# Kernel tuning notes

Measured on AMD Instinct MI355X. Metric: run time of the kernel, lower is better.

Reference implementation:

```python
import jax, jax.numpy as jnp
import numpy as np

N = 100000      # nodes
E = 3200000     # edges (avg degree 32)
F_IN = 16       # node_feature_size
R1, R2, R3 = 8, 16, 8   # gcn hidden sizes
N1 = 32                  # mlp hidden


def _lin(k, fan_in, shape):
    s = 1.0 / np.sqrt(fan_in)
    return jax.random.uniform(k, shape, minval=-s, maxval=s, dtype=jnp.float32)


def setup_inputs() -> dict:
    key = jax.random.key(0)
    ks = jax.random.split(key, 16)
    x = jax.random.normal(ks[0], (N, F_IN), dtype=jnp.float32)
    edge_index = jax.random.randint(ks[1], (2, E), 0, N, dtype=jnp.int64)
    return {
        "x": x,
        "edge_index": edge_index,
        # GraphConv k: out = mean_agg(x_j) @ W_rel + b + x @ W_root  (PyG GraphConv, lin_root bias=False)
        "W_rel1": _lin(ks[2], F_IN, (F_IN, R1)), "b1": _lin(ks[3], F_IN, (R1,)), "W_root1": _lin(ks[4], F_IN, (F_IN, R1)),
        "W_rel2": _lin(ks[5], R1, (R1, R2)),   "b2": _lin(ks[6], R1, (R2,)),   "W_root2": _lin(ks[7], R1, (R1, R2)),
        "W_rel3": _lin(ks[8], R2, (R2, R3)),   "b3": _lin(ks[9], R2, (R3,)),   "W_root3": _lin(ks[10], R2, (R2, R3)),
        "fc1_W": _lin(ks[11], R3, (R3, N1)), "fc1_b": _lin(ks[12], R3, (N1,)),
        "fc2_W": _lin(ks[13], N1, (N1, 1)),  "fc2_b": _lin(ks[14], N1, (1,)),
    }


def _graph_conv(x, src, dst, W_rel, b, W_root):
    # message: gather source features; aggregate: mean over incoming edges at dst
    n = x.shape[0]
    msg_sum = jax.ops.segment_sum(x[src], dst, num_segments=n)          # [N, F]
    cnt = jax.ops.segment_sum(jnp.ones(src.shape, x.dtype), dst, num_segments=n)
    mean = msg_sum / jnp.maximum(cnt, 1.0)[:, None]
    return mean @ W_rel + b + x @ W_root


def reference(x, edge_index, W_rel1, b1, W_root1, W_rel2, b2, W_root2,
              W_rel3, b3, W_root3, fc1_W, fc1_b, fc2_W, fc2_b):
    src, dst = edge_index[0], edge_index[1]
    h = jax.nn.sigmoid(_graph_conv(x, src, dst, W_rel1, b1, W_root1))
    h = jax.nn.sigmoid(_graph_conv(h, src, dst, W_rel2, b2, W_root2))
    h = jax.nn.sigmoid(_graph_conv(h, src, dst, W_rel3, b3, W_root3))
    h = jax.nn.sigmoid(h @ fc1_W + fc1_b)
    return h @ fc2_W + fc2_b   # [N, 1]
```

## Files before the change

kernel.cpp:

```cpp
#include <hip/hip_runtime.h>
#include <math.h>


#define CHUNK  8192
#define BW     128
#define MAXB   6144
#define MAXNB  800
#define MAXBLK 512

typedef _Float16 half8 __attribute__((ext_vector_type(8)));

static __device__ __forceinline__ float sigmoidf_(float x) {
    return 1.0f / (1.0f + expf(-x));
}

static __device__ __forceinline__ int scan256_excl(int v, int* s) {
    int tid = threadIdx.x;
    s[tid] = v;
    for (int off = 1; off < 256; off <<= 1) {
        __syncthreads();
        int t = (tid >= off) ? s[tid - off] : 0;
        __syncthreads();
        s[tid] += t;
    }
    __syncthreads();
    return s[tid] - v;
}

static __device__ __forceinline__ void gather_mean8(
    const half8* __restrict__ t, const int* __restrict__ csr,
    int rs, int d, float* s) {
#pragma unroll
    for (int c = 0; c < 8; ++c) s[c] = 0.0f;
    int e = 0;
    for (; e + 4 <= d; e += 4) {
        int4 ci = *(const int4*)(csr + rs + e);
        half8 v0 = t[ci.x]; half8 v1 = t[ci.y];
        half8 v2 = t[ci.z]; half8 v3 = t[ci.w];
#pragma unroll
        for (int c = 0; c < 8; ++c)
            s[c] += ((float)v0[c] + (float)v1[c]) + ((float)v2[c] + (float)v3[c]);
    }
    for (; e < d; ++e) {
        half8 v = t[csr[rs + e]];
#pragma unroll
        for (int c = 0; c < 8; ++c) s[c] += (float)v[c];
    }
    float inv = 1.0f / (float)(d > 0 ? d : 1);
#pragma unroll
    for (int c = 0; c < 8; ++c) s[c] *= inv;
}

__global__ __launch_bounds__(256)
void transform1_kernel(const float* __restrict__ x, const float* __restrict__ Wrel,
                       const float* __restrict__ bias, const float* __restrict__ Wroot,
                       _Float16* __restrict__ t1, _Float16* __restrict__ z1, int n) {
    __shared__ float sWr[128], sWo[128], sb[8];
    int tid = threadIdx.x;
    if (tid < 128) { sWr[tid] = Wrel[tid]; sWo[tid] = Wroot[tid]; }
    if (tid < 8) sb[tid] = bias[tid];
    __syncthreads();
    int node = blockIdx.x * 256 + tid;
    if (node >= n) return;
    const float4* x4 = (const float4*)x;
    float xv[16];
#pragma unroll
    for (int k = 0; k < 4; ++k) {
        float4 v = x4[node * 4 + k];
        xv[4 * k] = v.x; xv[4 * k + 1] = v.y; xv[4 * k + 2] = v.z; xv[4 * k + 3] = v.w;
    }
    float ta[8], za[8];
#pragma unroll
    for (int j = 0; j < 8; ++j) { ta[j] = 0.0f; za[j] = sb[j]; }
#pragma unroll
    for (int f = 0; f < 16; ++f) {
        float xf = xv[f];
#pragma unroll
        for (int j = 0; j < 8; ++j) {
            ta[j] += xf * sWr[f * 8 + j];
            za[j] += xf * sWo[f * 8 + j];
        }
    }
    half8 th, zh;
#pragma unroll
    for (int j = 0; j < 8; ++j) { th[j] = (_Float16)ta[j]; zh[j] = (_Float16)za[j]; }
    ((half8*)t1)[node] = th;
    ((half8*)z1)[node] = zh;
}

__global__ __launch_bounds__(256)
void bin_sort_kernel(const int* __restrict__ src, const int* __restrict__ dst,
                     unsigned* __restrict__ packed, int* __restrict__ counts_bm,
                     int* __restrict__ lstart_bm, int E, int NB) {
    __shared__ int s_hist[MAXNB];
    __shared__ int s_cur[MAXNB];
    __shared__ unsigned s_pk[CHUNK];
    __shared__ int s_scan[256];
    int tid = threadIdx.x, blk = blockIdx.x;
    for (int i = tid; i < NB; i += 256) s_hist[i] = 0;
    __syncthreads();

    int base = blk * CHUNK;
    int cnt = E - base; if (cnt > CHUNK) cnt = CHUNK;

    if (cnt == CHUNK) {
        const int4* d4 = (const int4*)(dst + base);
#pragma unroll
        for (int k = 0; k < CHUNK / 1024; ++k) {
            int4 d = d4[k * 256 + tid];
            atomicAdd(&s_hist[d.x >> 7], 1);
            atomicAdd(&s_hist[d.y >> 7], 1);
            atomicAdd(&s_hist[d.z >> 7], 1);
            atomicAdd(&s_hist[d.w >> 7], 1);
        }
    } else {
        for (int i = tid; i < cnt; i += 256) atomicAdd(&s_hist[dst[base + i] >> 7], 1);
    }
    __syncthreads();

    int per = (NB + 255) / 256;
    int st = tid * per;
    int lsum = 0;
    for (int j = 0; j < per; ++j)
        if (st + j < NB) lsum += s_hist[st + j];
    int excl = scan256_excl(lsum, s_scan);
    int run = excl;
    for (int j = 0; j < per; ++j)
        if (st + j < NB) { s_cur[st + j] = run; run += s_hist[st + j]; }
    __syncthreads();

    if (cnt == CHUNK) {
        const int4* d4 = (const int4*)(dst + base);
        const int4* s4 = (const int4*)(src + base);
#pragma unroll
        for (int k = 0; k < CHUNK / 1024; ++k) {
            int4 d = d4[k * 256 + tid];
            int4 s = s4[k * 256 + tid];
            int dd[4] = {d.x, d.y, d.z, d.w};
            int ss[4] = {s.x, s.y, s.z, s.w};
#pragma unroll
            for (int j = 0; j < 4; ++j) {
                int pos = atomicAdd(&s_cur[dd[j] >> 7], 1);
                s_pk[pos] = ((unsigned)(dd[j] & 127) << 17) | (unsigned)ss[j];
            }
        }
    } else {
        for (int i = tid; i < cnt; i += 256) {
            int d = dst[base + i], s = src[base + i];
            int pos = atomicAdd(&s_cur[d >> 7], 1);
            s_pk[pos] = ((unsigned)(d & 127) << 17) | (unsigned)s;
        }
    }
    __syncthreads();

    for (int i = tid; i < cnt; i += 256) packed[base + i] = s_pk[i];
    for (int i = tid; i < NB; i += 256) {
        int h = s_hist[i];
        counts_bm[blk * NB + i] = h;
        lstart_bm[blk * NB + i] = s_cur[i] - h;
    }
}

__global__ __launch_bounds__(256)
void transpose2_kernel(const int* __restrict__ a, int* __restrict__ at,
                       const int* __restrict__ b, int* __restrict__ bt,
                       int rows, int cols) {
    __shared__ int ta[32][33];
    __shared__ int tb[32][33];
    int tx = threadIdx.x & 31, ty = threadIdx.x >> 5;
    int r0 = blockIdx.y * 32, c0 = blockIdx.x * 32;
#pragma unroll
    for (int k = 0; k < 4; ++k) {
        int r = r0 + ty + 8 * k, c = c0 + tx;
        if (r < rows && c < cols) {
            ta[ty + 8 * k][tx] = a[r * cols + c];
            tb[ty + 8 * k][tx] = b[r * cols + c];
        }
    }
    __syncthreads();
#pragma unroll
    for (int k = 0; k < 4; ++k) {
        int c = c0 + ty + 8 * k, r = r0 + tx;
        if (c < cols && r < rows) {
            at[c * rows + r] = ta[tx][ty + 8 * k];
            bt[c * rows + r] = tb[tx][ty + 8 * k];
        }
    }
}

__global__ __launch_bounds__(256)
void btot_kernel(const int* __restrict__ counts_t, int* __restrict__ btot, int NBLK) {
    __shared__ int s_scan[256];
    int b = blockIdx.x, tid = threadIdx.x;
    int v = 0;
    for (int i = tid; i < NBLK; i += 256) v += counts_t[b * NBLK + i];
    scan256_excl(v, s_scan);
    if (tid == 255) btot[b] = s_scan[255];
}

__global__ __launch_bounds__(1024)
void bscan_kernel(const int* __restrict__ btot, int* __restrict__ bstart, int NB) {
    __shared__ int lds[1024];
    int tid = threadIdx.x;
    int v = (tid < NB) ? (((btot[tid] + 3) & ~3) + 512) : 0;
    lds[tid] = v;
    for (int off = 1; off < 1024; off <<= 1) {
        __syncthreads();
        int t = (tid >= off) ? lds[tid - off] : 0;
        __syncthreads();
        lds[tid] += t;
    }
    __syncthreads();
    if (tid < NB) bstart[tid] = lds[tid] - v;
}

__global__ __launch_bounds__(256)
void bucket_sort_kernel(const unsigned* __restrict__ packed,
                        const int* __restrict__ counts_t,
                        const int* __restrict__ lstart_t,
                        const int* __restrict__ bstart,
                        int* __restrict__ csr_src, int* __restrict__ deg,
                        int* __restrict__ rowstart, int N, int NB, int NBLK) {
    __shared__ int s_cnt[MAXBLK], s_lst[MAXBLK], s_off[MAXBLK];
    __shared__ unsigned s_p[MAXB];
    __shared__ int s_out[MAXB];
    __shared__ int h[BW], hs[BW], curb[BW];
    __shared__ int s_scan[256];
    __shared__ int s_tot, s_ptot;
    int b = blockIdx.x, tid = threadIdx.x;
    int beg = bstart[b];

    for (int i = tid; i < NBLK; i += 256) {
        s_cnt[i] = counts_t[b * NBLK + i];
        s_lst[i] = lstart_t[b * NBLK + i];
    }
    __syncthreads();

    int per = (NBLK + 255) / 256;
    int st = tid * per;
    int lsum = 0;
    for (int j = 0; j < per; ++j)
        if (st + j < NBLK) lsum += s_cnt[st + j];
    int excl = scan256_excl(lsum, s_scan);
    if (tid == 255) s_tot = s_scan[255];
    int run = excl;
    for (int j = 0; j < per; ++j)
        if (st + j < NBLK) { s_off[st + j] = run; run += s_cnt[st + j]; }
    __syncthreads();
    int cnt = s_tot; if (cnt > MAXB) cnt = MAXB;

    for (int blk = tid; blk < NBLK; blk += 256) {
        int c = s_cnt[blk], o = s_off[blk];
        const unsigned* p = packed + (size_t)blk * CHUNK + s_lst[blk];
        for (int j = 0; j < c; ++j) s_p[o + j] = p[j];
    }
    if (tid < BW) h[tid] = 0;
    __syncthreads();

    for (int i = tid; i < cnt; i += 256) atomicAdd(&h[s_p[i] >> 17], 1);
    __syncthreads();
    if (tid == 0) {
        int acc = 0;
        for (int i = 0; i < BW; ++i) { hs[i] = acc; acc += (h[i] + 3) & ~3; }
        s_ptot = acc;
    }
    __syncthreads();
    if (tid < BW) {
        curb[tid] = hs[tid];
        int node = b * BW + tid;
        if (node < N) { deg[node] = h[tid]; rowstart[node] = beg + hs[tid]; }
    }
    __syncthreads();
    for (int i = tid; i < cnt; i += 256) {
        unsigned p = s_p[i];
        int pos = atomicAdd(&curb[p >> 17], 1);
        s_out[pos] = (int)(p & 0x1FFFF);
    }
    __syncthreads();
    int ptot = s_ptot; if (ptot > MAXB) ptot = MAXB;
    for (int i = tid; i < ptot; i += 256) csr_src[beg + i] = s_out[i];
}

__global__ __launch_bounds__(256)
void agg1_kernel(const _Float16* __restrict__ t1, const _Float16* __restrict__ z1,
                 const int* __restrict__ rowstart, const int* __restrict__ deg,
                 const int* __restrict__ csr, _Float16* __restrict__ h1, int n) {
    int node = blockIdx.x * 256 + threadIdx.x;
    if (node >= n) return;
    float s[8];
    gather_mean8((const half8*)t1, csr, rowstart[node], deg[node], s);
    half8 z = ((const half8*)z1)[node];
    half8 o;
#pragma unroll
    for (int c = 0; c < 8; ++c) o[c] = (_Float16)sigmoidf_(s[c] + (float)z[c]);
    ((half8*)h1)[node] = o;
}

__global__ __launch_bounds__(256)
void gcn2_fused_kernel(const _Float16* __restrict__ h1,
                       const int* __restrict__ rowstart, const int* __restrict__ deg,
                       const int* __restrict__ csr,
                       const float* __restrict__ W2r, const float* __restrict__ b2,
                       const float* __restrict__ W2o,
                       const float* __restrict__ W3r, const float* __restrict__ b3,
                       const float* __restrict__ W3o,
                       _Float16* __restrict__ t3, _Float16* __restrict__ z3, int n) {
    __shared__ float sW2r[128], sW2o[128], sW3r[128], sW3o[128], sb2[16], sb3[8];
    int tid = threadIdx.x;
    if (tid < 128) {
        sW2r[tid] = W2r[tid]; sW2o[tid] = W2o[tid];
        sW3r[tid] = W3r[tid]; sW3o[tid] = W3o[tid];
    }
    if (tid < 16) sb2[tid] = b2[tid];
    if (tid < 8) sb3[tid] = b3[tid];
    __syncthreads();
    int node = blockIdx.x * 256 + tid;
    if (node >= n) return;

    float m[8];
    gather_mean8((const half8*)h1, csr, rowstart[node], deg[node], m);
    half8 sf = ((const half8*)h1)[node];
    float x8[8];
#pragma unroll
    for (int c = 0; c < 8; ++c) x8[c] = (float)sf[c];

    float v16[16];
#pragma unroll
    for (int j = 0; j < 16; ++j) {
        float a = sb2[j];
#pragma unroll
        for (int f = 0; f < 8; ++f)
            a += m[f] * sW2r[f * 16 + j] + x8[f] * sW2o[f * 16 + j];
        v16[j] = sigmoidf_(a);
    }
    float ta[8], za[8];
#pragma unroll
    for (int j = 0; j < 8; ++j) { ta[j] = 0.0f; za[j] = sb3[j]; }
#pragma unroll
    for (int f = 0; f < 16; ++f) {
        float hv = v16[f];
#pragma unroll
        for (int j = 0; j < 8; ++j) {
            ta[j] += hv * sW3r[f * 8 + j];
            za[j] += hv * sW3o[f * 8 + j];
        }
    }
    half8 th, zh;
#pragma unroll
    for (int j = 0; j < 8; ++j) { th[j] = (_Float16)ta[j]; zh[j] = (_Float16)za[j]; }
    ((half8*)t3)[node] = th;
    ((half8*)z3)[node] = zh;
}

__global__ __launch_bounds__(256)
void agg3_mlp_kernel(const _Float16* __restrict__ t3, const _Float16* __restrict__ z3,
                     const int* __restrict__ rowstart, const int* __restrict__ deg,
                     const int* __restrict__ csr,
                     const float* __restrict__ fc1W, const float* __restrict__ fc1b,
                     const float* __restrict__ fc2W, const float* __restrict__ fc2b,
                     float* __restrict__ out, int n) {
    __shared__ float sW1[256], sb1[32], sW2[32];
    __shared__ float sb2_;
    int tid = threadIdx.x;
    if (tid < 256) sW1[tid] = fc1W[tid];
    if (tid < 32) { sb1[tid] = fc1b[tid]; sW2[tid] = fc2W[tid]; }
    if (tid == 0) sb2_ = fc2b[0];
    __syncthreads();
    int node = blockIdx.x * 256 + tid;
    if (node >= n) return;

    float s[8];
    gather_mean8((const half8*)t3, csr, rowstart[node], deg[node], s);
    half8 z = ((const half8*)z3)[node];
    float h[8];
#pragma unroll
    for (int c = 0; c < 8; ++c) h[c] = sigmoidf_(s[c] + (float)z[c]);

    float acc = sb2_;
#pragma unroll
    for (int j = 0; j < 32; ++j) {
        float a = sb1[j];
#pragma unroll
        for (int f = 0; f < 8; ++f) a += h[f] * sW1[f * 32 + j];
        acc += sW2[j] * sigmoidf_(a);
    }
    out[node] = acc;
}

extern "C" void kernel_launch(void* const* d_in, const int* in_sizes, int n_in,
                              void* d_out, int out_size, void* d_ws, size_t ws_size,
                              hipStream_t stream) {
    const float* x      = (const float*)d_in[0];
    const int*   ei     = (const int*)d_in[1];
    const float* Wrel1  = (const float*)d_in[2];
    const float* b1     = (const float*)d_in[3];
    const float* Wroot1 = (const float*)d_in[4];
    const float* Wrel2  = (const float*)d_in[5];
    const float* b2     = (const float*)d_in[6];
    const float* Wroot2 = (const float*)d_in[7];
    const float* Wrel3  = (const float*)d_in[8];
    const float* b3     = (const float*)d_in[9];
    const float* Wroot3 = (const float*)d_in[10];
    const float* fc1W   = (const float*)d_in[11];
    const float* fc1b   = (const float*)d_in[12];
    const float* fc2W   = (const float*)d_in[13];
    const float* fc2b   = (const float*)d_in[14];
    float* out = (float*)d_out;

    const int N = in_sizes[0] / 16;
    const int E = in_sizes[1] / 2;
    const int* e_src = ei;
    const int* e_dst = ei + E;

    const int NB   = (N + BW - 1) / BW;
    const int NBLK = (E + CHUNK - 1) / CHUNK;

    char* ws = (char*)d_ws;
    size_t off = 0;
    auto alloc = [&](size_t bytes) { char* p = ws + off; off += (bytes + 15) & ~size_t(15); return p; };
    unsigned* packed   = (unsigned*)alloc((size_t)NBLK * CHUNK * 4);
    int* counts_bm     = (int*)alloc((size_t)NBLK * NB * 4);
    int* lstart_bm     = (int*)alloc((size_t)NBLK * NB * 4);
    int* counts_t      = (int*)alloc((size_t)NBLK * NB * 4);
    int* lstart_t      = (int*)alloc((size_t)NBLK * NB * 4);
    int* btot          = (int*)alloc((size_t)NB * 4);
    int* bstart        = (int*)alloc((size_t)NB * 4);
    int* csr_src       = (int*)alloc(((size_t)E + (size_t)NB * 516) * 4);
    int* deg           = (int*)alloc((size_t)N * 4);
    int* rowstart      = (int*)alloc((size_t)N * 4);
    _Float16* t1       = (_Float16*)alloc((size_t)N * 8 * 2);
    _Float16* z1       = (_Float16*)alloc((size_t)N * 8 * 2);
    _Float16* h1       = (_Float16*)alloc((size_t)N * 8 * 2);
    _Float16* t3       = (_Float16*)alloc((size_t)N * 8 * 2);
    _Float16* z3       = (_Float16*)alloc((size_t)N * 8 * 2);

    const int nbN = (N + 255) / 256;

    transform1_kernel<<<nbN, 256, 0, stream>>>(x, Wrel1, b1, Wroot1, t1, z1, N);

    bin_sort_kernel<<<NBLK, 256, 0, stream>>>(e_src, e_dst, packed, counts_bm, lstart_bm, E, NB);
    dim3 tgrid((NB + 31) / 32, (NBLK + 31) / 32);
    transpose2_kernel<<<tgrid, 256, 0, stream>>>(counts_bm, counts_t, lstart_bm, lstart_t, NBLK, NB);
    btot_kernel<<<NB, 256, 0, stream>>>(counts_t, btot, NBLK);
    bscan_kernel<<<1, 1024, 0, stream>>>(btot, bstart, NB);
    bucket_sort_kernel<<<NB, 256, 0, stream>>>(packed, counts_t, lstart_t, bstart,
                                               csr_src, deg, rowstart, N, NB, NBLK);

    agg1_kernel<<<nbN, 256, 0, stream>>>(t1, z1, rowstart, deg, csr_src, h1, N);
    gcn2_fused_kernel<<<nbN, 256, 0, stream>>>(h1, rowstart, deg, csr_src,
                                               Wrel2, b2, Wroot2, Wrel3, b3, Wroot3, t3, z3, N);
    agg3_mlp_kernel<<<nbN, 256, 0, stream>>>(t3, z3, rowstart, deg, csr_src,
                                             fc1W, fc1b, fc2W, fc2b, out, N);
}
```

Measured before the change: 232.0 us.

## Fuse graph-build preamble: merge transform into bin sort, drop transpose and scan kernels

Folds the first-layer feature transform into the bin-sort kernel, replaces the transpose, per-bucket total and bucket-scan kernels with global atomics into btot, and has each bucket-sort block compute its own start offset by scanning btot. Per-chunk bucket segments are padded to multiples of four in a wider packed stride so the bucket sort can copy with uint4 loads. The goal is fewer kernel launches and less intermediate traffic. In exchange there is a memset, strided (uncoalesced) reads of counts_bm and lstart_bm, and redundant prefix work in every bucket-sort block.

```diff
diff --git a/kernel.cpp b/kernel.cpp
--- a/kernel.cpp
+++ b/kernel.cpp
@@ -3,6 +3,7 @@
 
 
 #define CHUNK  8192
+#define PSTR   10752
 #define BW     128
 #define MAXB   6144
 #define MAXNB  800
@@ -52,53 +53,56 @@
 }
 
 __global__ __launch_bounds__(256)
-void transform1_kernel(const float* __restrict__ x, const float* __restrict__ Wrel,
-                       const float* __restrict__ bias, const float* __restrict__ Wroot,
-                       _Float16* __restrict__ t1, _Float16* __restrict__ z1, int n) {
-    __shared__ float sWr[128], sWo[128], sb[8];
-    int tid = threadIdx.x;
-    if (tid < 128) { sWr[tid] = Wrel[tid]; sWo[tid] = Wroot[tid]; }
-    if (tid < 8) sb[tid] = bias[tid];
-    __syncthreads();
-    int node = blockIdx.x * 256 + tid;
-    if (node >= n) return;
-    const float4* x4 = (const float4*)x;
-    float xv[16];
-#pragma unroll
-    for (int k = 0; k < 4; ++k) {
-        float4 v = x4[node * 4 + k];
-        xv[4 * k] = v.x; xv[4 * k + 1] = v.y; xv[4 * k + 2] = v.z; xv[4 * k + 3] = v.w;
-    }
-    float ta[8], za[8];
-#pragma unroll
-    for (int j = 0; j < 8; ++j) { ta[j] = 0.0f; za[j] = sb[j]; }
-#pragma unroll
-    for (int f = 0; f < 16; ++f) {
-        float xf = xv[f];
-#pragma unroll
-        for (int j = 0; j < 8; ++j) {
-            ta[j] += xf * sWr[f * 8 + j];
-            za[j] += xf * sWo[f * 8 + j];
-        }
-    }
-    half8 th, zh;
-#pragma unroll
-    for (int j = 0; j < 8; ++j) { th[j] = (_Float16)ta[j]; zh[j] = (_Float16)za[j]; }
-    ((half8*)t1)[node] = th;
-    ((half8*)z1)[node] = zh;
-}
-
-__global__ __launch_bounds__(256)
-void bin_sort_kernel(const int* __restrict__ src, const int* __restrict__ dst,
+void bin_sort_kernel(const float* __restrict__ x, const float* __restrict__ W1r,
+                     const float* __restrict__ b1v, const float* __restrict__ W1o,
+                     _Float16* __restrict__ t1, _Float16* __restrict__ z1,
+                     const int* __restrict__ src, const int* __restrict__ dst,
                      unsigned* __restrict__ packed, int* __restrict__ counts_bm,
-                     int* __restrict__ lstart_bm, int E, int NB) {
+                     int* __restrict__ lstart_bm, int* __restrict__ btot,
+                     int E, int N, int NB, int NBLK) {
     __shared__ int s_hist[MAXNB];
     __shared__ int s_cur[MAXNB];
-    __shared__ unsigned s_pk[CHUNK];
+    __shared__ unsigned s_pk[PSTR];
     __shared__ int s_scan[256];
+    __shared__ float sW[264];
     int tid = threadIdx.x, blk = blockIdx.x;
+
+    if (tid < 128) { sW[tid] = W1r[tid]; sW[128 + tid] = W1o[tid]; }
+    if (tid < 8) sW[256 + tid] = b1v[tid];
     for (int i = tid; i < NB; i += 256) s_hist[i] = 0;
     __syncthreads();
+    {
+        int node = blk * 256 + tid;
+        if (node < N) {
+            const float4* x4 = (const float4*)x;
+            float xv[16];
+#pragma unroll
+            for (int k = 0; k < 4; ++k) {
+                float4 v = x4[node * 4 + k];
+                xv[4 * k] = v.x; xv[4 * k + 1] = v.y;
+                xv[4 * k + 2] = v.z; xv[4 * k + 3] = v.w;
+            }
+            float ta[8], za[8];
+#pragma unroll
+            for (int j = 0; j < 8; ++j) { ta[j] = 0.0f; za[j] = sW[256 + j]; }
+#pragma unroll
+            for (int f = 0; f < 16; ++f) {
+                float xf = xv[f];
+#pragma unroll
+                for (int j = 0; j < 8; ++j) {
+                    ta[j] += xf * sW[f * 8 + j];
+                    za[j] += xf * sW[128 + f * 8 + j];
+                }
+            }
+            half8 th, zh;
+#pragma unroll
+            for (int j = 0; j < 8; ++j) { th[j] = (_Float16)ta[j]; zh[j] = (_Float16)za[j]; }
+            ((half8*)t1)[node] = th;
+            ((half8*)z1)[node] = zh;
+        }
+    }
+
+    if (blk >= NBLK) return;
 
     int base = blk * CHUNK;
     int cnt = E - base; if (cnt > CHUNK) cnt = CHUNK;
@@ -122,11 +126,12 @@
     int st = tid * per;
     int lsum = 0;
     for (int j = 0; j < per; ++j)
-        if (st + j < NB) lsum += s_hist[st + j];
+        if (st + j < NB) lsum += (s_hist[st + j] + 3) & ~3;
     int excl = scan256_excl(lsum, s_scan);
+    int padtot = s_scan[255];
     int run = excl;
     for (int j = 0; j < per; ++j)
-        if (st + j < NB) { s_cur[st + j] = run; run += s_hist[st + j]; }
+        if (st + j < NB) { s_cur[st + j] = run; run += (s_hist[st + j] + 3) & ~3; }
     __syncthreads();
 
     if (cnt == CHUNK) {
@@ -153,72 +158,20 @@
     }
     __syncthreads();
 
-    for (int i = tid; i < cnt; i += 256) packed[base + i] = s_pk[i];
+    for (int i = tid; i < padtot; i += 256) packed[(size_t)blk * PSTR + i] = s_pk[i];
     for (int i = tid; i < NB; i += 256) {
         int h = s_hist[i];
         counts_bm[blk * NB + i] = h;
         lstart_bm[blk * NB + i] = s_cur[i] - h;
-    }
-}
-
-__global__ __launch_bounds__(256)
-void transpose2_kernel(const int* __restrict__ a, int* __restrict__ at,
-                       const int* __restrict__ b, int* __restrict__ bt,
-                       int rows, int cols) {
-    __shared__ int ta[32][33];
-    __shared__ int tb[32][33];
-    int tx = threadIdx.x & 31, ty = threadIdx.x >> 5;
-    int r0 = blockIdx.y * 32, c0 = blockIdx.x * 32;
-#pragma unroll
-    for (int k = 0; k < 4; ++k) {
-        int r = r0 + ty + 8 * k, c = c0 + tx;
-        if (r < rows && c < cols) {
-            ta[ty + 8 * k][tx] = a[r * cols + c];
-            tb[ty + 8 * k][tx] = b[r * cols + c];
-        }
-    }
-    __syncthreads();
-#pragma unroll
-    for (int k = 0; k < 4; ++k) {
-        int c = c0 + ty + 8 * k, r = r0 + tx;
-        if (c < cols && r < rows) {
-            at[c * rows + r] = ta[tx][ty + 8 * k];
-            bt[c * rows + r] = tb[tx][ty + 8 * k];
-        }
-    }
-}
-
-__global__ __launch_bounds__(256)
-void btot_kernel(const int* __restrict__ counts_t, int* __restrict__ btot, int NBLK) {
-    __shared__ int s_scan[256];
-    int b = blockIdx.x, tid = threadIdx.x;
-    int v = 0;
-    for (int i = tid; i < NBLK; i += 256) v += counts_t[b * NBLK + i];
-    scan256_excl(v, s_scan);
-    if (tid == 255) btot[b] = s_scan[255];
-}
-
-__global__ __launch_bounds__(1024)
-void bscan_kernel(const int* __restrict__ btot, int* __restrict__ bstart, int NB) {
-    __shared__ int lds[1024];
-    int tid = threadIdx.x;
-    int v = (tid < NB) ? (((btot[tid] + 3) & ~3) + 512) : 0;
-    lds[tid] = v;
-    for (int off = 1; off < 1024; off <<= 1) {
-        __syncthreads();
-        int t = (tid >= off) ? lds[tid - off] : 0;
-        __syncthreads();
-        lds[tid] += t;
-    }
-    __syncthreads();
-    if (tid < NB) bstart[tid] = lds[tid] - v;
+        if (h) atomicAdd(&btot[i], h);
+    }
 }
 
 __global__ __launch_bounds__(256)
 void bucket_sort_kernel(const unsigned* __restrict__ packed,
-                        const int* __restrict__ counts_t,
-                        const int* __restrict__ lstart_t,
-                        const int* __restrict__ bstart,
+                        const int* __restrict__ counts_bm,
+                        const int* __restrict__ lstart_bm,
+                        const int* __restrict__ btot,
                         int* __restrict__ csr_src, int* __restrict__ deg,
                         int* __restrict__ rowstart, int N, int NB, int NBLK) {
     __shared__ int s_cnt[MAXBLK], s_lst[MAXBLK], s_off[MAXBLK];
@@ -228,11 +181,15 @@
     __shared__ int s_scan[256];
     __shared__ int s_tot, s_ptot;
     int b = blockIdx.x, tid = threadIdx.x;
-    int beg = bstart[b];
+
+    int partial = 0;
+    for (int i = tid; i < b; i += 256) partial += ((btot[i] + 3) & ~3) + 512;
+    scan256_excl(partial, s_scan);
+    int beg = s_scan[255];
 
     for (int i = tid; i < NBLK; i += 256) {
-        s_cnt[i] = counts_t[b * NBLK + i];
-        s_lst[i] = lstart_t[b * NBLK + i];
+        s_cnt[i] = counts_bm[i * NB + b];
+        s_lst[i] = lstart_bm[i * NB + b];
     }
     __syncthreads();
 
@@ -251,8 +208,15 @@
 
     for (int blk = tid; blk < NBLK; blk += 256) {
         int c = s_cnt[blk], o = s_off[blk];
-        const unsigned* p = packed + (size_t)blk * CHUNK + s_lst[blk];
-        for (int j = 0; j < c; ++j) s_p[o + j] = p[j];
+        const uint4* p = (const uint4*)(packed + (size_t)blk * PSTR + s_lst[blk]);
+        for (int j = 0; j < c; j += 4) {
+            uint4 v = p[j >> 2];
+            int r = c - j;
+            s_p[o + j] = v.x;
+            if (r > 1) s_p[o + j + 1] = v.y;
+            if (r > 2) s_p[o + j + 2] = v.z;
+            if (r > 3) s_p[o + j + 3] = v.w;
+        }
     }
     if (tid < BW) h[tid] = 0;
     __syncthreads();
@@ -414,17 +378,15 @@
 
     const int NB   = (N + BW - 1) / BW;
     const int NBLK = (E + CHUNK - 1) / CHUNK;
+    const int nbN  = (N + 255) / 256;
 
     char* ws = (char*)d_ws;
     size_t off = 0;
     auto alloc = [&](size_t bytes) { char* p = ws + off; off += (bytes + 15) & ~size_t(15); return p; };
-    unsigned* packed   = (unsigned*)alloc((size_t)NBLK * CHUNK * 4);
+    unsigned* packed   = (unsigned*)alloc((size_t)NBLK * PSTR * 4);
     int* counts_bm     = (int*)alloc((size_t)NBLK * NB * 4);
     int* lstart_bm     = (int*)alloc((size_t)NBLK * NB * 4);
-    int* counts_t      = (int*)alloc((size_t)NBLK * NB * 4);
-    int* lstart_t      = (int*)alloc((size_t)NBLK * NB * 4);
     int* btot          = (int*)alloc((size_t)NB * 4);
-    int* bstart        = (int*)alloc((size_t)NB * 4);
     int* csr_src       = (int*)alloc(((size_t)E + (size_t)NB * 516) * 4);
     int* deg           = (int*)alloc((size_t)N * 4);
     int* rowstart      = (int*)alloc((size_t)N * 4);
@@ -434,18 +396,14 @@
     _Float16* t3       = (_Float16*)alloc((size_t)N * 8 * 2);
     _Float16* z3       = (_Float16*)alloc((size_t)N * 8 * 2);
 
-    const int nbN = (N + 255) / 256;
-
-    transform1_kernel<<<nbN, 256, 0, stream>>>(x, Wrel1, b1, Wroot1, t1, z1, N);
-
-    bin_sort_kernel<<<NBLK, 256, 0, stream>>>(e_src, e_dst, packed, counts_bm, lstart_bm, E, NB);
-    dim3 tgrid((NB + 31) / 32, (NBLK + 31) / 32);
-    transpose2_kernel<<<tgrid, 256, 0, stream>>>(counts_bm, counts_t, lstart_bm, lstart_t, NBLK, NB);
-    btot_kernel<<<NB, 256, 0, stream>>>(counts_t, btot, NBLK);
-    bscan_kernel<<<1, 1024, 0, stream>>>(btot, bstart, NB);
-    bucket_sort_kernel<<<NB, 256, 0, stream>>>(packed, counts_t, lstart_t, bstart,
+    hipMemsetAsync(btot, 0, (size_t)NB * 4, stream);
+
+    const int gbuild = (NBLK > nbN) ? NBLK : nbN;
+    bin_sort_kernel<<<gbuild, 256, 0, stream>>>(
+        x, Wrel1, b1, Wroot1, t1, z1, e_src, e_dst,
+        packed, counts_bm, lstart_bm, btot, E, N, NB, NBLK);
+    bucket_sort_kernel<<<NB, 256, 0, stream>>>(packed, counts_bm, lstart_bm, btot,
                                                csr_src, deg, rowstart, N, NB, NBLK);
-
     agg1_kernel<<<nbN, 256, 0, stream>>>(t1, z1, rowstart, deg, csr_src, h1, N);
     gcn2_fused_kernel<<<nbN, 256, 0, stream>>>(h1, rowstart, deg, csr_src,
                                                Wrel2, b2, Wroot2, Wrel3, b3, Wroot3, t3, z3, N);
```

New measurement: 234.9 us. Within noise of the previous version (+1.3%).
